# Kernel tuning notes

Hardware: AMD Instinct MI355X
Metric: run time of the kernel (lower is better)

## Reference

```python
import jax, jax.numpy as jnp
import numpy as np
import math

N, CIN, COUT, K, H, W = 16, 512, 512, 1024, 64, 64


def setup_inputs() -> dict:
    key = jax.random.key(0)
    k0, k1, k2, k3, k4 = jax.random.split(key, 5)
    latent = jax.random.normal(k0, (N, CIN, H, W), dtype=jnp.float32)
    # kaiming_uniform_ on (K, COUT): bound = sqrt(6 / fan_in), fan_in = COUT
    cb_bound = math.sqrt(6.0 / COUT)
    codebook = jax.random.uniform(k1, (K, COUT), minval=-cb_bound, maxval=cb_bound, dtype=jnp.float32)
    # nn.Linear default init: uniform(-1/sqrt(fan_in), 1/sqrt(fan_in)), weight stored (out, in)
    wq = jax.random.uniform(k2, (COUT, CIN), minval=-1 / math.sqrt(CIN), maxval=1 / math.sqrt(CIN), dtype=jnp.float32)
    wk = jax.random.uniform(k3, (COUT, COUT), minval=-1 / math.sqrt(COUT), maxval=1 / math.sqrt(COUT), dtype=jnp.float32)
    wv = jax.random.uniform(k4, (COUT, COUT), minval=-1 / math.sqrt(COUT), maxval=1 / math.sqrt(COUT), dtype=jnp.float32)
    return {"latent": latent, "codebook": codebook, "wq": wq, "wk": wk, "wv": wv, "temperature": 1}


def _forward(latent, codebook, wq, wk, wv, temperature):
    n, cin, h, w = latent.shape
    kk, cout = codebook.shape
    scale = math.sqrt(cin)

    q = jnp.einsum("nchw,oc->nhwo", latent, wq)          # [n,h,w,cout]
    kmat = codebook @ wk.T                                   # [k,cout]
    v = codebook @ wv.T                                      # [k,cout]
    logit = jnp.einsum("nhwc,kc->nhwk", q, kmat) / scale  # [n,h,w,k]

    # ---- no-grad mask / histogram computation (dropout branch) ----
    lg = jax.lax.stop_gradient(logit)
    rk = jax.random.key(1234)
    r1, r2, r3 = jax.random.split(rk, 3)
    prob = jax.nn.softmax(lg, axis=-1)
    prob = jnp.where(prob < 1.0 / kk, 0.0, prob)
    mask = jax.random.bernoulli(r1, prob)                    # [n,h,w,k] bool
    trueCode = jnp.argmax(prob, axis=-1)                     # [n,h,w] int
    flat = trueCode.reshape(n, -1)
    binCount = jnp.zeros((n, kk), dtype=jnp.float32).at[jnp.arange(n)[:, None], flat].add(1.0)
    frequency = binCount[jnp.arange(n)[:, None, None], trueCode]  # [n,h,w]
    dropout = jax.random.bernoulli(r2, frequency / float(h * w))   # [n,h,w] bool
    scatterMask = jax.nn.one_hot(trueCode, kk, dtype=jnp.bool_) & dropout[..., None]
    mask = mask | scatterMask

    maskedLogit = jnp.where(mask, -1e9, logit)

    # ---- hard gumbel-softmax (straight-through) ----
    g = jax.random.gumbel(r3, maskedLogit.shape, dtype=maskedLogit.dtype)
    y_soft = jax.nn.softmax((maskedLogit + g) / temperature, axis=-1)
    y_hard = jax.nn.one_hot(jnp.argmax(y_soft, axis=-1), kk, dtype=y_soft.dtype)
    sample = y_hard - jax.lax.stop_gradient(y_soft) + y_soft

    result = jnp.einsum("nhwk,kc->nhwc", sample, v)
    quantized = jnp.transpose(result, (0, 3, 1, 2))          # [n,cout,h,w]
    code = jnp.argmax(sample, axis=-1)
    return quantized, code, logit, trueCode, frequency, binCount


def reference(latent, codebook, wq, wk, wv, temperature):
    return _forward(latent, codebook, wq, wk, wv, temperature)
```

## Files before the change

kernel.cpp:

```cpp
#include <hip/hip_runtime.h>
#include <stdint.h>
#include <stddef.h>

#define NB   16
#define CIN  512
#define COUT 512
#define KK   1024

#define MARGIN    2e-5f
#define INV_SCALE 0.04419417382415922f

typedef short short4v __attribute__((ext_vector_type(4)));
typedef short short8v __attribute__((ext_vector_type(8)));
typedef float f32x4  __attribute__((ext_vector_type(4)));

union Frag { short4v h[2]; short8v v8; };

__host__ __device__ inline void tf2x32(uint32_t k0, uint32_t k1,
                                       uint32_t x0, uint32_t x1,
                                       uint32_t& o0, uint32_t& o1) {
  uint32_t ks2 = k0 ^ k1 ^ 0x1BD11BDAu;
  x0 += k0; x1 += k1;
#define TF_RND(r) { x0 += x1; x1 = (x1 << r) | (x1 >> (32 - r)); x1 ^= x0; }
  TF_RND(13) TF_RND(15) TF_RND(26) TF_RND(6)
  x0 += k1;  x1 += ks2 + 1u;
  TF_RND(17) TF_RND(29) TF_RND(16) TF_RND(24)
  x0 += ks2; x1 += k0 + 2u;
  TF_RND(13) TF_RND(15) TF_RND(26) TF_RND(6)
  x0 += k0;  x1 += k1 + 3u;
  TF_RND(17) TF_RND(29) TF_RND(16) TF_RND(24)
  x0 += k1;  x1 += ks2 + 4u;
  TF_RND(13) TF_RND(15) TF_RND(26) TF_RND(6)
  x0 += ks2; x1 += k0 + 5u;
#undef TF_RND
  o0 = x0; o1 = x1;
}

__device__ inline float bits_to_u(uint32_t b) {
  return __uint_as_float((b >> 9) | 0x3f800000u) - 1.0f;
}

__device__ __host__ inline uint16_t f2bf(float f) {
  union { float f; uint32_t u; } c; c.f = f;
  uint32_t r = (c.u + 0x7fffu + ((c.u >> 16) & 1u)) >> 16;
  return (uint16_t)r;
}
__device__ inline float bf2f(uint16_t h) {
  union { uint32_t u; float f; } c; c.u = ((uint32_t)h) << 16;
  return c.f;
}

__device__ inline int permpos(int c) {
  const int base32 = c & ~31, within = c & 31;
  const int g = (within >> 2) & 3;
  const int e = (within & 16) ? (4 + (within & 3)) : (within & 3);
  return base32 + g * 8 + e;
}

__global__ __launch_bounds__(256) void k_prep(const float* __restrict__ cb,
                                              const float* __restrict__ wk,
                                              const float* __restrict__ wv,
                                              double* __restrict__ kmatT64,
                                              float* __restrict__ v) {
  __shared__ __align__(16) float rows[8][CIN];
  const int k0 = blockIdx.x * 8;
  const int t = threadIdx.x;
#pragma unroll
  for (int kk = 0; kk < 8; ++kk)
    for (int c = t; c < CIN; c += 256) rows[kk][c] = cb[(size_t)(k0 + kk) * CIN + c];
  __syncthreads();
#pragma unroll
  for (int oo = 0; oo < 2; ++oo) {
    const int o = t + oo * 256;
    const float* kr = wk + (size_t)o * CIN;
    const float* vr = wv + (size_t)o * CIN;
    double ak[8] = {0,0,0,0,0,0,0,0}, av[8] = {0,0,0,0,0,0,0,0};
    for (int c = 0; c < CIN; c += 4) {
      const float4 k4 = *(const float4*)(kr + c);
      const float4 v4 = *(const float4*)(vr + c);
#pragma unroll
      for (int kk = 0; kk < 8; ++kk) {
        const float4 c4 = *(const float4*)&rows[kk][c];
        ak[kk] += (double)c4.x * (double)k4.x + (double)c4.y * (double)k4.y
                + (double)c4.z * (double)k4.z + (double)c4.w * (double)k4.w;
        av[kk] += (double)c4.x * (double)v4.x + (double)c4.y * (double)v4.y
                + (double)c4.z * (double)v4.z + (double)c4.w * (double)v4.w;
      }
    }
#pragma unroll
    for (int kk = 0; kk < 8; ++kk) {
      kmatT64[(size_t)o * KK + k0 + kk] = ak[kk];
      v[(size_t)(k0 + kk) * COUT + o]  = (float)av[kk];
    }
  }
}

__global__ __launch_bounds__(256) void k_wfold(const float* __restrict__ wq,
                                               const double* __restrict__ kmatT64,
                                               double* __restrict__ WT64,
                                               uint16_t* __restrict__ Wph,
                                               uint16_t* __restrict__ Wpl) {
  __shared__ __align__(16) float  As[16][64];
  __shared__ __align__(16) double Bs[16][128];
  const int t  = threadIdx.x;
  const int cb = (blockIdx.x >> 3) * 64;
  const int kb = (blockIdx.x & 7) * 128;
  const int tc = t >> 4, tk = t & 15;

  double acc[4][8];
#pragma unroll
  for (int i = 0; i < 4; ++i)
#pragma unroll
    for (int j = 0; j < 8; ++j) acc[i][j] = 0.0;

  for (int o0 = 0; o0 < COUT; o0 += 16) {
    {
      const int o2 = t >> 4, c4 = (t & 15) * 4;
      float4 f = *(const float4*)&wq[(size_t)(o0 + o2) * CIN + cb + c4];
      As[o2][c4+0] = f.x; As[o2][c4+1] = f.y; As[o2][c4+2] = f.z; As[o2][c4+3] = f.w;
    }
    {
      const int o2 = t >> 4, k8 = (t & 15) * 8;
      const double* src = &kmatT64[(size_t)(o0 + o2) * KK + kb + k8];
#pragma unroll
      for (int j = 0; j < 8; ++j) Bs[o2][k8 + j] = src[j];
    }
    __syncthreads();
#pragma unroll 4
    for (int o2 = 0; o2 < 16; ++o2) {
      double a[4], b[8];
#pragma unroll
      for (int i = 0; i < 4; ++i) a[i] = (double)As[o2][tc*4 + i];
#pragma unroll
      for (int j = 0; j < 8; ++j) b[j] = Bs[o2][tk*8 + j];
#pragma unroll
      for (int i = 0; i < 4; ++i)
#pragma unroll
        for (int j = 0; j < 8; ++j) acc[i][j] += a[i] * b[j];
    }
    __syncthreads();
  }
#pragma unroll
  for (int i = 0; i < 4; ++i) {
    const int c = cb + tc*4 + i;
    const int pp = permpos(c);
#pragma unroll
    for (int j = 0; j < 8; ++j) {
      const int k = kb + tk*8 + j;
      const double a = acc[i][j];
      WT64[(size_t)k * CIN + c] = a;
      const float wf = (float)a;
      const uint16_t hb = f2bf(wf);
      const float lof = wf - bf2f(hb);
      Wph[(size_t)k * CIN + pp] = hb;
      Wpl[(size_t)k * CIN + pp] = f2bf(lof);
    }
  }
}

__global__ __launch_bounds__(256) void k_aprep(const float* __restrict__ latent,
                                               uint16_t* __restrict__ Apk) {
  __shared__ float T[128][68];
  const int rb = blockIdx.x, n = rb >> 6, h = rb & 63, t = threadIdx.x;
  for (int c0 = 0; c0 < 512; c0 += 128) {
    const int c2 = t >> 1, wh = (t & 1) * 32;
    const float* src = latent + (size_t)n * 2097152 + (size_t)(c0 + c2) * 4096 + h * 64 + wh;
#pragma unroll
    for (int i = 0; i < 8; ++i)
      *(float4*)&T[c2][wh + i*4] = *(const float4*)(src + i*4);
    __syncthreads();
    const int w = t & 63, cp = t >> 6;
    const int cs = (c0 >> 5) + cp;
    const int p = rb * 64 + w;
    uint16_t* dst = Apk + ((size_t)cs * 65536 + p) * 64;
#pragma unroll
    for (int q = 0; q < 8; ++q) {
      short8v vv;
#pragma unroll
      for (int j = 0; j < 4; ++j) {
        const float f = T[cp*32 + (q & 3) * 4 + (q >> 2) * 16 + j][w];
        const uint16_t hb = f2bf(f);
        vv[j]     = (short)hb;
        vv[4 + j] = (short)f2bf(f - bf2f(hb));
      }
      *(short8v*)(dst + q * 8) = vv;
    }
    __syncthreads();
  }
}

#define STAGE_B(buf_, st_) do {                                            \
  const int kc_ = (st_) >> 4, cs_ = (st_) & 15;                            \
  _Pragma("unroll")                                                        \
  for (int i_ = 0; i_ < 4; ++i_) {                                         \
    const int half_ = i_ >> 1;                                             \
    const int D_ = (i_ & 1) * 8192 + t * 16;                               \
    const int kcol_ = D_ >> 6;                                             \
    const int bs_ = ((D_ >> 4) & 3) ^ ((kcol_ >> 1) & 3);                  \
    const uint16_t* gsrc_ = (half_ ? Wpl : Wph) +                          \
        ((size_t)(kc_ * 256 + kcol_) * 512 + cs_ * 32 + bs_ * 8);          \
    uint16_t* ldst_ = &Bst[buf_][half_ * 8192 + (D_ >> 1)];                \
    __builtin_amdgcn_global_load_lds(                                      \
        (const __attribute__((address_space(1))) uint32_t*)gsrc_,          \
        (__attribute__((address_space(3))) uint32_t*)ldst_, 16, 0, 0);     \
  } } while (0)

#define STAGE_A(buf_, st_) do {                                            \
  const int cs_ = (st_) & 15;                                              \
  _Pragma("unroll")                                                        \
  for (int i_ = 0; i_ < 2; ++i_) {                                         \
    const int D_ = i_ * 8192 + t * 16;                                     \
    const int row_ = D_ >> 7;                                              \
    const int q_ = ((D_ >> 4) & 7) ^ (row_ & 7);                           \
    const uint16_t* gsrc_ = Apk +                                          \
        ((size_t)cs_ * 65536 + pbase + row_) * 64 + q_ * 8;                \
    uint16_t* ldst_ = &Ast[buf_][D_ >> 1];                                 \
    __builtin_amdgcn_global_load_lds(                                      \
        (const __attribute__((address_space(1))) uint32_t*)gsrc_,          \
        (__attribute__((address_space(3))) uint32_t*)ldst_, 16, 0, 0);     \
  } } while (0)

__global__ __launch_bounds__(512, 1) void k_logit(
    const uint16_t* __restrict__ Apk,
    const uint16_t* __restrict__ Wph, const uint16_t* __restrict__ Wpl,
    const float* __restrict__ latent, const double* __restrict__ WT64,
    float* __restrict__ out_logit, int* __restrict__ trueCode, int* __restrict__ binCnt) {
  __shared__ __align__(16) char smem[98304];
  uint16_t (*Bst)[16384] = (uint16_t(*)[16384])smem;
  uint16_t (*Ast)[8192]  = (uint16_t(*)[8192])(smem + 65536);
  float* rowBv   = (float*)(smem + 65536);
  int*   rowBk   = (int*)  (smem + 65536 + 512);
  int*   candCnt = (int*)  (smem + 65536 + 1024);
  int  (*candK)[8] = (int(*)[8])(smem + 65536 + 1536);

  const int t = threadIdx.x;
  const int wave = t >> 6, lane = t & 63;
  const int wr = wave >> 2, wc = wave & 3;
  const int rb = blockIdx.x;
  const int n = rb >> 5;
  const int pbase = rb * 128;
  const int lg = lane >> 4, l15 = lane & 15;

  float bestv[4][4]; int bestk[4][4];
#pragma unroll
  for (int rt = 0; rt < 4; ++rt)
#pragma unroll
    for (int reg = 0; reg < 4; ++reg) { bestv[rt][reg] = -1.0e30f; bestk[rt][reg] = 0; }

  f32x4 acc[4][4];

  STAGE_A(0, 0);
  STAGE_B(0, 0);
  __syncthreads();

  for (int st = 0; st < 64; ++st) {
    const int cur = st & 1, kc = st >> 4, cs = st & 15;
    if (cs == 0) {
#pragma unroll
      for (int rt = 0; rt < 4; ++rt)
#pragma unroll
        for (int ct = 0; ct < 4; ++ct) acc[rt][ct] = (f32x4){0.f, 0.f, 0.f, 0.f};
    }
    if (st < 63) { STAGE_A(cur ^ 1, st + 1); STAGE_B(cur ^ 1, st + 1); }

    Frag ah[4], al[4];
#pragma unroll
    for (int rt = 0; rt < 4; ++rt) {
      const int row = wr * 64 + rt * 16 + l15;
      const uint16_t* ab = &Ast[cur][row * 64];
      const int s0 = (lg ^ (row & 7)) * 8;
      Frag f0, f1;
      f0.v8 = *(const short8v*)(ab + s0);
      f1.v8 = *(const short8v*)(ab + (s0 ^ 32));
      ah[rt].h[0] = f0.h[0]; ah[rt].h[1] = f1.h[0];
      al[rt].h[0] = f0.h[1]; al[rt].h[1] = f1.h[1];
    }

#pragma unroll
    for (int ct = 0; ct < 4; ++ct) {
      const int kcol = wc * 64 + ct * 16 + l15;
      const int sw = lg ^ ((kcol >> 1) & 3);
      Frag bh, bl;
      bh.v8 = *(const short8v*)&Bst[cur][kcol * 32 + sw * 8];
      bl.v8 = *(const short8v*)&Bst[cur][8192 + kcol * 32 + sw * 8];
#pragma unroll
      for (int rt = 0; rt < 4; ++rt) {
        acc[rt][ct] = __builtin_amdgcn_mfma_f32_16x16x32_bf16(ah[rt].v8, bh.v8, acc[rt][ct], 0, 0, 0);
        acc[rt][ct] = __builtin_amdgcn_mfma_f32_16x16x32_bf16(ah[rt].v8, bl.v8, acc[rt][ct], 0, 0, 0);
        acc[rt][ct] = __builtin_amdgcn_mfma_f32_16x16x32_bf16(al[rt].v8, bh.v8, acc[rt][ct], 0, 0, 0);
      }
    }
    if (cs == 15) {
#pragma unroll
      for (int rt = 0; rt < 4; ++rt) {
#pragma unroll
        for (int reg = 0; reg < 4; ++reg) {
          const int prow = pbase + wr * 64 + rt * 16 + 4 * lg + reg;
          float* dst = out_logit + (size_t)prow * KK + kc * 256 + wc * 64 + l15;
#pragma unroll
          for (int ct = 0; ct < 4; ++ct) {
            const float v = acc[rt][ct][reg] * INV_SCALE;
            dst[ct * 16] = v;
            if (v > bestv[rt][reg]) { bestv[rt][reg] = v; bestk[rt][reg] = kc * 256 + wc * 64 + ct * 16 + l15; }
          }
        }
      }
    }
    __syncthreads();
  }

#pragma unroll
  for (int rt = 0; rt < 4; ++rt)
#pragma unroll
    for (int reg = 0; reg < 4; ++reg) {
      float v = bestv[rt][reg]; int k = bestk[rt][reg];
#pragma unroll
      for (int off = 1; off < 16; off <<= 1) {
        const float ov = __shfl_xor(v, off);
        const int   ok = __shfl_xor(k, off);
        if (ov > v || (ov == v && ok < k)) { v = ov; k = ok; }
      }
      bestv[rt][reg] = v; bestk[rt][reg] = k;
    }
  if (t < 128) candCnt[t] = 0;
  if (wc == 0 && l15 == 0) {
#pragma unroll
    for (int rt = 0; rt < 4; ++rt)
#pragma unroll
      for (int reg = 0; reg < 4; ++reg) {
        const int r = wr * 64 + rt * 16 + 4 * lg + reg;
        rowBv[r] = bestv[rt][reg]; rowBk[r] = bestk[rt][reg];
      }
  }
  __syncthreads();
#pragma unroll
  for (int m = 1; m < 4; ++m) {
    if (wc == m && l15 == 0) {
#pragma unroll
      for (int rt = 0; rt < 4; ++rt)
#pragma unroll
        for (int reg = 0; reg < 4; ++reg) {
          const int r = wr * 64 + rt * 16 + 4 * lg + reg;
          const float v = bestv[rt][reg]; const int k = bestk[rt][reg];
          if (v > rowBv[r] || (v == rowBv[r] && k < rowBk[r])) { rowBv[r] = v; rowBk[r] = k; }
        }
    }
    __syncthreads();
  }

  {
    const int r = t >> 2, qd = t & 3;
    const size_t base = (size_t)(pbase + r) * KK + qd * 256;
    const float thr = rowBv[r] - MARGIN;
    for (int x = 0; x < 64; ++x) {
      const float4 f = *(const float4*)&out_logit[base + x * 4];
      const int kb = qd * 256 + x * 4;
      if (f.x >= thr) { int id = atomicAdd(&candCnt[r], 1); if (id < 8) candK[r][id] = kb + 0; }
      if (f.y >= thr) { int id = atomicAdd(&candCnt[r], 1); if (id < 8) candK[r][id] = kb + 1; }
      if (f.z >= thr) { int id = atomicAdd(&candCnt[r], 1); if (id < 8) candK[r][id] = kb + 2; }
      if (f.w >= thr) { int id = atomicAdd(&candCnt[r], 1); if (id < 8) candK[r][id] = kb + 3; }
    }
  }
  __syncthreads();

  const int wv = t >> 6, lane_ = t & 63;
  for (int rr = 0; rr < 16; ++rr) {
    const int r = wv * 16 + rr;
    const int p = pbase + r;
    int cnt = candCnt[r]; if (cnt > 8) cnt = 8;
    if (cnt <= 1) {
      if (lane_ == 0) {
        const int tc0 = rowBk[r];
        trueCode[p] = tc0;
        atomicAdd(&binCnt[n * KK + tc0], 1);
      }
    } else {
      const float* Ap = latent + (size_t)(p >> 12) * 2097152 + (p & 4095);
      int ks[8];
#pragma unroll
      for (int m = 0; m < 8; ++m) ks[m] = candK[r][m < cnt ? m : 0];
      double part[8] = {0, 0, 0, 0, 0, 0, 0, 0};
#pragma unroll
      for (int jj = 0; jj < 8; ++jj) {
        const int c = jj * 64 + lane_;
        const double lv = (double)Ap[(size_t)c * 4096];
#pragma unroll
        for (int m = 0; m < 8; ++m)
          if (m < cnt) part[m] += lv * WT64[(size_t)ks[m] * CIN + c];
      }
#pragma unroll
      for (int m = 0; m < 8; ++m)
        for (int off = 32; off; off >>= 1) part[m] += __shfl_xor(part[m], off);
      if (lane_ == 0) {
        double bv = -1.0e300; int bkk = KK;
#pragma unroll
        for (int m = 0; m < 8; ++m)
          if (m < cnt && (part[m] > bv || (part[m] == bv && ks[m] < bkk))) { bv = part[m]; bkk = ks[m]; }
        trueCode[p] = bkk;
        atomicAdd(&binCnt[n * KK + bkk], 1);
      }
    }
  }
}

__global__ __launch_bounds__(256) void k_final(const float* __restrict__ logit,
                                               const int* __restrict__ trueCode,
                                               const int* __restrict__ binCnt,
                                               float* __restrict__ out_code,
                                               float* __restrict__ out_tc,
                                               float* __restrict__ out_freq,
                                               int* __restrict__ code_int,
                                               uint32_t r1a, uint32_t r1b,
                                               uint32_t r2a, uint32_t r2b,
                                               uint32_t r3a, uint32_t r3b) {
  const int lane = threadIdx.x & 63;
  const int p = blockIdx.x * 4 + (threadIdx.x >> 6);
  const float* Lr = logit + (size_t)p * KK + lane * 16;

  float l[16];
#pragma unroll
  for (int i = 0; i < 4; ++i) {
    const float4 f = *(const float4*)(Lr + i * 4);
    l[i*4+0] = f.x; l[i*4+1] = f.y; l[i*4+2] = f.z; l[i*4+3] = f.w;
  }

  float m = l[0];
#pragma unroll
  for (int i = 1; i < 16; ++i) m = fmaxf(m, l[i]);
  for (int off = 32; off; off >>= 1) m = fmaxf(m, __shfl_xor(m, off));

  float e[16], s = 0.f;
#pragma unroll
  for (int i = 0; i < 16; ++i) { e[i] = __expf(l[i] - m); s += e[i]; }
  for (int off = 32; off; off >>= 1) s += __shfl_xor(s, off);

  const int tc = trueCode[p];
  const float fq = (float)binCnt[(p >> 12) * KK + tc];
  uint32_t d0, d1; tf2x32(r2a, r2b, 0u, (uint32_t)p, d0, d1);
  const bool drop = bits_to_u(d0 ^ d1) < fq * (1.0f / 4096.0f);

  const float thr = s * 0.0009765625f;
  float bv = -3.0e38f; int bk = 0;
#pragma unroll
  for (int j = 0; j < 16; ++j) {
    const int k = lane * 16 + j;
    const uint32_t idx = (uint32_t)(p * KK + k);
    uint32_t m0, m1, g0, g1;
    tf2x32(r1a, r1b, 0u, idx, m0, m1);
    tf2x32(r3a, r3b, 0u, idx, g0, g1);
    const bool mk = ((e[j] >= thr) && (bits_to_u(m0 ^ m1) * s < e[j])) || (k == tc && drop);
    const float u3  = fmaxf(bits_to_u(g0 ^ g1), 1.17549435082228751e-38f);
    const float gum = -__logf(-logf(u3));
    const float z = mk ? (gum - 1.0e9f) : (l[j] + gum);
    if (z > bv) { bv = z; bk = k; }
  }
  for (int off = 32; off; off >>= 1) {
    const float ov = __shfl_xor(bv, off);
    const int   ok = __shfl_xor(bk, off);
    if (ov > bv || (ov == bv && ok < bk)) { bv = ov; bk = ok; }
  }
  if (lane == 0) {
    out_code[p] = (float)bk; code_int[p] = bk;
    out_tc[p] = (float)tc;   out_freq[p] = fq;
  }
}

__global__ __launch_bounds__(256) void k_quant(const float* __restrict__ v,
                                               const int* __restrict__ code_int,
                                               float* __restrict__ outq) {
  const int rb = blockIdx.x;
  const int n = rb >> 6, h = rb & 63;
  const int t = threadIdx.x;
  __shared__ int codes[64];
  if (t < 64) codes[t] = code_int[rb * 64 + t];
  __syncthreads();
  const int w = t & 63, og = t >> 6;
  const float* vr = v + (size_t)codes[w] * COUT;
  float* ob = outq + (size_t)n * COUT * 4096 + (size_t)h * 64 + w;
  for (int o = og * 128; o < og * 128 + 128; ++o)
    ob[(size_t)o * 4096] = vr[o];
}

__global__ __launch_bounds__(256) void k_bincopy(const int* __restrict__ binCnt,
                                                 float* __restrict__ outb) {
  const int i = blockIdx.x * 256 + threadIdx.x;
  if (i < NB * KK) outb[i] = (float)binCnt[i];
}

extern "C" void kernel_launch(void* const* d_in, const int* in_sizes, int n_in,
                              void* d_out, int out_size, void* d_ws, size_t ws_size,
                              hipStream_t stream) {
  const float* latent   = (const float*)d_in[0];
  const float* codebook = (const float*)d_in[1];
  const float* wq       = (const float*)d_in[2];
  const float* wk       = (const float*)d_in[3];
  const float* wv       = (const float*)d_in[4];

  float* out = (float*)d_out;
  float* out_quant = out;
  float* out_code  = out + 33554432;
  float* out_logit = out + 33619968;
  float* out_tc    = out + 100728832;
  float* out_freq  = out + 100794368;
  float* out_bin   = out + 100859904;

  double*   WT64 = (double*)  out_quant;
  uint16_t* Wph  = (uint16_t*)(out_quant + 1048576);
  uint16_t* Wpl  = (uint16_t*)(out_quant + 1310720);

  char* ws = (char*)d_ws;
  uint16_t* Apk     = (uint16_t*)(ws);
  double*   kmatT64 = (double*)(ws);
  float*    v       = (float*)(ws + 134217728);
  int*      trueCode= (int*)  (ws + 136314880);
  int*      code_int= (int*)  (ws + 136577024);
  int*      binCnt  = (int*)  (ws + 136839168);

  uint32_t r1a, r1b, r2a, r2b, r3a, r3b;
  tf2x32(0u, 1234u, 0u, 0u, r1a, r1b);
  tf2x32(0u, 1234u, 0u, 1u, r2a, r2b);
  tf2x32(0u, 1234u, 0u, 2u, r3a, r3b);

  hipMemsetAsync(binCnt, 0, NB * KK * sizeof(int), stream);
  k_prep  <<<128,   256, 0, stream>>>(codebook, wk, wv, kmatT64, v);
  k_wfold <<<64,    256, 0, stream>>>(wq, kmatT64, WT64, Wph, Wpl);
  k_aprep <<<1024,  256, 0, stream>>>(latent, Apk);
  k_logit <<<512,   512, 0, stream>>>(Apk, Wph, Wpl, latent, WT64,
                                      out_logit, trueCode, binCnt);
  k_final <<<16384, 256, 0, stream>>>(out_logit, trueCode, binCnt,
                                      out_code, out_tc, out_freq, code_int,
                                      r1a, r1b, r2a, r2b, r3a, r3b);
  k_quant <<<1024,  256, 0, stream>>>(v, code_int, out_quant);
  k_bincopy<<<64,   256, 0, stream>>>(binCnt, out_bin);
}
```

Measured before the change: 964.1 us.

## Compute two codebook chunks per A tile and restructure prefetch pipeline

The logit GEMM now handles two 256-column codebook chunks per stage, using a second set of accumulators. This halves the number of times each A tile is reloaded into LDS and halves the loop trip count. The pipeline is reworked so stage loads are issued two iterations ahead, using explicit vmcnt waits and raw barriers instead of __syncthreads, with LDS grown to 160KB. Launch bounds change to 2 blocks per CU, which will not fit given the LDS size. Those bounds also cap registers while the accumulator count doubles, which risks spilling.

```diff
diff --git a/kernel.cpp b/kernel.cpp
--- a/kernel.cpp
+++ b/kernel.cpp
@@ -189,24 +189,22 @@
   }
 }
 
-#define STAGE_B(buf_, st_) do {                                            \
-  const int kc_ = (st_) >> 4, cs_ = (st_) & 15;                            \
+#define STAGE(buf_, st_) do {                                              \
+  const int kcp_ = (st_) >> 4, cs_ = (st_) & 15;                           \
   _Pragma("unroll")                                                        \
-  for (int i_ = 0; i_ < 4; ++i_) {                                         \
-    const int half_ = i_ >> 1;                                             \
-    const int D_ = (i_ & 1) * 8192 + t * 16;                               \
+  for (int i_ = 0; i_ < 8; ++i_) {                                         \
+    const int j_ = i_ >> 2, ii_ = i_ & 3;                                  \
+    const int half_ = ii_ >> 1;                                            \
+    const int D_ = (ii_ & 1) * 8192 + t * 16;                              \
     const int kcol_ = D_ >> 6;                                             \
     const int bs_ = ((D_ >> 4) & 3) ^ ((kcol_ >> 1) & 3);                  \
     const uint16_t* gsrc_ = (half_ ? Wpl : Wph) +                          \
-        ((size_t)(kc_ * 256 + kcol_) * 512 + cs_ * 32 + bs_ * 8);          \
-    uint16_t* ldst_ = &Bst[buf_][half_ * 8192 + (D_ >> 1)];                \
+        ((size_t)((kcp_ * 2 + j_) * 256 + kcol_) * 512 + cs_ * 32 + bs_ * 8); \
+    char* ldst_ = smem + (buf_) * 65536 + j_ * 32768 + half_ * 16384 + D_; \
     __builtin_amdgcn_global_load_lds(                                      \
         (const __attribute__((address_space(1))) uint32_t*)gsrc_,          \
         (__attribute__((address_space(3))) uint32_t*)ldst_, 16, 0, 0);     \
-  } } while (0)
-
-#define STAGE_A(buf_, st_) do {                                            \
-  const int cs_ = (st_) & 15;                                              \
+  }                                                                        \
   _Pragma("unroll")                                                        \
   for (int i_ = 0; i_ < 2; ++i_) {                                         \
     const int D_ = i_ * 8192 + t * 16;                                     \
@@ -214,24 +212,28 @@
     const int q_ = ((D_ >> 4) & 7) ^ (row_ & 7);                           \
     const uint16_t* gsrc_ = Apk +                                          \
         ((size_t)cs_ * 65536 + pbase + row_) * 64 + q_ * 8;                \
-    uint16_t* ldst_ = &Ast[buf_][D_ >> 1];                                 \
+    char* ldst_ = smem + 131072 + (buf_) * 16384 + D_;                     \
     __builtin_amdgcn_global_load_lds(                                      \
         (const __attribute__((address_space(1))) uint32_t*)gsrc_,          \
         (__attribute__((address_space(3))) uint32_t*)ldst_, 16, 0, 0);     \
   } } while (0)
 
-__global__ __launch_bounds__(512, 1) void k_logit(
+#define BARRIER() do { __builtin_amdgcn_sched_barrier(0);                  \
+  __builtin_amdgcn_s_barrier(); __builtin_amdgcn_sched_barrier(0); } while (0)
+#define WAITV10() do { __builtin_amdgcn_sched_barrier(0);                  \
+  asm volatile("s_waitcnt vmcnt(10)" ::: "memory");                        \
+  __builtin_amdgcn_sched_barrier(0); } while (0)
+
+__global__ __launch_bounds__(512, 2) void k_logit(
     const uint16_t* __restrict__ Apk,
     const uint16_t* __restrict__ Wph, const uint16_t* __restrict__ Wpl,
     const float* __restrict__ latent, const double* __restrict__ WT64,
     float* __restrict__ out_logit, int* __restrict__ trueCode, int* __restrict__ binCnt) {
-  __shared__ __align__(16) char smem[98304];
-  uint16_t (*Bst)[16384] = (uint16_t(*)[16384])smem;
-  uint16_t (*Ast)[8192]  = (uint16_t(*)[8192])(smem + 65536);
-  float* rowBv   = (float*)(smem + 65536);
-  int*   rowBk   = (int*)  (smem + 65536 + 512);
-  int*   candCnt = (int*)  (smem + 65536 + 1024);
-  int  (*candK)[8] = (int(*)[8])(smem + 65536 + 1536);
+  __shared__ __align__(16) char smem[163840];
+  float* rowBv   = (float*)(smem + 131072);
+  int*   rowBk   = (int*)  (smem + 131072 + 512);
+  int*   candCnt = (int*)  (smem + 131072 + 1024);
+  int  (*candK)[8] = (int(*)[8])(smem + 131072 + 1536);
 
   const int t = threadIdx.x;
   const int wave = t >> 6, lane = t & 63;
@@ -247,27 +249,30 @@
 #pragma unroll
     for (int reg = 0; reg < 4; ++reg) { bestv[rt][reg] = -1.0e30f; bestk[rt][reg] = 0; }
 
-  f32x4 acc[4][4];
-
-  STAGE_A(0, 0);
-  STAGE_B(0, 0);
-  __syncthreads();
-
-  for (int st = 0; st < 64; ++st) {
-    const int cur = st & 1, kc = st >> 4, cs = st & 15;
+  f32x4 acc[2][4][4];
+
+  STAGE(0, 0);
+  STAGE(1, 1);
+
+  for (int st = 0; st < 32; ++st) {
+    const int cur = st & 1, kcp = st >> 4, cs = st & 15;
+    WAITV10();
+    BARRIER();
     if (cs == 0) {
 #pragma unroll
-      for (int rt = 0; rt < 4; ++rt)
-#pragma unroll
-        for (int ct = 0; ct < 4; ++ct) acc[rt][ct] = (f32x4){0.f, 0.f, 0.f, 0.f};
-    }
-    if (st < 63) { STAGE_A(cur ^ 1, st + 1); STAGE_B(cur ^ 1, st + 1); }
-
+      for (int j = 0; j < 2; ++j)
+#pragma unroll
+        for (int rt = 0; rt < 4; ++rt)
+#pragma unroll
+          for (int ct = 0; ct < 4; ++ct) acc[j][rt][ct] = (f32x4){0.f, 0.f, 0.f, 0.f};
+    }
+
+    const uint16_t* Ab = (const uint16_t*)(smem + 131072 + cur * 16384);
     Frag ah[4], al[4];
 #pragma unroll
     for (int rt = 0; rt < 4; ++rt) {
       const int row = wr * 64 + rt * 16 + l15;
-      const uint16_t* ab = &Ast[cur][row * 64];
+      const uint16_t* ab = Ab + row * 64;
       const int s0 = (lg ^ (row & 7)) * 8;
       Frag f0, f1;
       f0.v8 = *(const short8v*)(ab + s0);
@@ -277,36 +282,48 @@
     }
 
 #pragma unroll
-    for (int ct = 0; ct < 4; ++ct) {
-      const int kcol = wc * 64 + ct * 16 + l15;
-      const int sw = lg ^ ((kcol >> 1) & 3);
-      Frag bh, bl;
-      bh.v8 = *(const short8v*)&Bst[cur][kcol * 32 + sw * 8];
-      bl.v8 = *(const short8v*)&Bst[cur][8192 + kcol * 32 + sw * 8];
-#pragma unroll
-      for (int rt = 0; rt < 4; ++rt) {
-        acc[rt][ct] = __builtin_amdgcn_mfma_f32_16x16x32_bf16(ah[rt].v8, bh.v8, acc[rt][ct], 0, 0, 0);
-        acc[rt][ct] = __builtin_amdgcn_mfma_f32_16x16x32_bf16(ah[rt].v8, bl.v8, acc[rt][ct], 0, 0, 0);
-        acc[rt][ct] = __builtin_amdgcn_mfma_f32_16x16x32_bf16(al[rt].v8, bh.v8, acc[rt][ct], 0, 0, 0);
-      }
-    }
+    for (int j = 0; j < 2; ++j) {
+      const uint16_t* Bb = (const uint16_t*)(smem + cur * 65536 + j * 32768);
+#pragma unroll
+      for (int ct = 0; ct < 4; ++ct) {
+        const int kcol = wc * 64 + ct * 16 + l15;
+        const int sw = lg ^ ((kcol >> 1) & 3);
+        Frag bh, bl;
+        bh.v8 = *(const short8v*)(Bb + kcol * 32 + sw * 8);
+        bl.v8 = *(const short8v*)(Bb + 8192 + kcol * 32 + sw * 8);
+#pragma unroll
+        for (int rt = 0; rt < 4; ++rt) {
+          acc[j][rt][ct] = __builtin_amdgcn_mfma_f32_16x16x32_bf16(ah[rt].v8, bh.v8, acc[j][rt][ct], 0, 0, 0);
+          acc[j][rt][ct] = __builtin_amdgcn_mfma_f32_16x16x32_bf16(ah[rt].v8, bl.v8, acc[j][rt][ct], 0, 0, 0);
+          acc[j][rt][ct] = __builtin_amdgcn_mfma_f32_16x16x32_bf16(al[rt].v8, bh.v8, acc[j][rt][ct], 0, 0, 0);
+        }
+      }
+    }
+
     if (cs == 15) {
 #pragma unroll
-      for (int rt = 0; rt < 4; ++rt) {
-#pragma unroll
-        for (int reg = 0; reg < 4; ++reg) {
-          const int prow = pbase + wr * 64 + rt * 16 + 4 * lg + reg;
-          float* dst = out_logit + (size_t)prow * KK + kc * 256 + wc * 64 + l15;
-#pragma unroll
-          for (int ct = 0; ct < 4; ++ct) {
-            const float v = acc[rt][ct][reg] * INV_SCALE;
-            dst[ct * 16] = v;
-            if (v > bestv[rt][reg]) { bestv[rt][reg] = v; bestk[rt][reg] = kc * 256 + wc * 64 + ct * 16 + l15; }
+      for (int j = 0; j < 2; ++j) {
+#pragma unroll
+        for (int rt = 0; rt < 4; ++rt) {
+#pragma unroll
+          for (int reg = 0; reg < 4; ++reg) {
+            const int prow = pbase + wr * 64 + rt * 16 + 4 * lg + reg;
+            float* dst = out_logit + (size_t)prow * KK + (kcp * 2 + j) * 256 + wc * 64 + l15;
+#pragma unroll
+            for (int ct = 0; ct < 4; ++ct) {
+              const float v = acc[j][rt][ct][reg] * INV_SCALE;
+              dst[ct * 16] = v;
+              if (v > bestv[rt][reg]) {
+                bestv[rt][reg] = v;
+                bestk[rt][reg] = (kcp * 2 + j) * 256 + wc * 64 + ct * 16 + l15;
+              }
+            }
           }
         }
       }
     }
-    __syncthreads();
+    BARRIER();
+    if (st + 2 < 32) STAGE(cur, st + 2);
   }
 
 #pragma unroll
```

Result: slower. 0.9995 ms (+3.7%).
